# Kernel tuning notes

Measured on AMD Instinct MI355X. Metric: run time of the kernel, lower is better.

## Reference

```python
import jax, jax.numpy as jnp
import numpy as np

MAX_SEQ_LEN = 2048
H, K = 16, 8
D_IN, D_OUT = 1024, 1024
D_H, D_O = D_IN // H, D_OUT // H


def _get_phi(L, K):
    # Hankel matrix Z[i,j] = 2 / ((i+j)^3 - (i+j) + 1e-7), 1-indexed
    e = np.arange(1, L + 1, dtype=np.float64)
    s = e[:, None] + e[None, :]
    Z = 2.0 / (s ** 3 - s + 1e-7)
    sigma, phi = np.linalg.eigh(Z)
    sigma, phi = sigma[-K:], phi[:, -K:]
    phi = phi * sigma ** 0.25
    return jnp.asarray(phi, dtype=jnp.float32)  # (L, K)


def setup_inputs() -> dict:
    key = jax.random.key(0)
    k_x, k_w, k_d = jax.random.split(key, 3)
    B, T = 4, 2048
    x = jax.random.normal(k_x, (B, T, D_IN), dtype=jnp.float32)
    # kaiming_uniform(a=sqrt(5)) on (H,K,d_h,d_o): fan_in = K*d_h*d_o, bound = 1/sqrt(fan_in)
    fan_in = K * D_H * D_O
    bound = 1.0 / np.sqrt(fan_in)
    weight = jax.random.uniform(k_w, (H, K, D_H, D_O), minval=-bound, maxval=bound, dtype=jnp.float32)
    # torch init is zeros; use small random so the score path is exercised
    diag = 0.02 * jax.random.normal(k_d, (K, D_IN), dtype=jnp.float32)
    phi = _get_phi(MAX_SEQ_LEN, K)
    return {"x": x, "weight": weight, "diag": diag, "phi": phi}


def reference(x, weight, diag, phi):
    B, T, _ = x.shape
    Hh, Kk, d_h, d_o = weight.shape
    # scores: (B, T, K) = phi[:T] broadcast + x @ diag^T
    scores = phi[:T][None, :, :] + jnp.einsum('bti,ki->btk', x, diag)
    xh = x.reshape(B, T, Hh, d_h).transpose(0, 2, 1, 3)  # (B, H, T, d_h)
    # per-head, per-expert GEMM -> (B, H, K, T, d_o)
    y = jnp.einsum('bhti,hkio->bhkto', xh, weight)
    # score-weighted combine over experts -> (B, T, H, d_o)
    y = jnp.einsum('bhkto,btk->btho', y, scores)
    return y.reshape(B, T, Hh * d_o)
```

## Files before the change

### kernel.cpp

```cpp
#include <hip/hip_runtime.h>
#include <hip/hip_bf16.h>

#define BT    8192
#define SEQ_T 2048
#define DIN   1024
#define NH    16
#define NK    8
#define DH    64
#define DO    64
#define TT    256

typedef __bf16 bf16;
typedef __attribute__((ext_vector_type(8))) __bf16 bf16x8;
typedef __attribute__((ext_vector_type(4))) __bf16 bf16x4;
typedef __attribute__((ext_vector_type(4))) float floatx4;

__device__ inline void async_load16(const void* g, void* l) {
  __builtin_amdgcn_global_load_lds(
      (const __attribute__((address_space(1))) unsigned int*)g,
      (__attribute__((address_space(3))) unsigned int*)l, 16, 0, 0);
}

__global__ __launch_bounds__(256) void prep_kernel(
    const float* __restrict__ x, const float* __restrict__ weight,
    const float* __restrict__ diag, const float* __restrict__ phi,
    float* __restrict__ scores_t, bf16* __restrict__ wt)
{
  int blk = blockIdx.x, tid = threadIdx.x;
  if (blk < BT / 4) {
    int wave = tid >> 6, lane = tid & 63;
    int token = blk * 4 + wave;
    const floatx4* xr = (const floatx4*)(x + (size_t)token * DIN);
    const floatx4* dg = (const floatx4*)diag;
    floatx4 acc[NK];
#pragma unroll
    for (int k = 0; k < NK; k++) acc[k] = (floatx4){0.f, 0.f, 0.f, 0.f};
#pragma unroll
    for (int it = 0; it < 4; it++) {
      floatx4 xv = xr[it * 64 + lane];
#pragma unroll
      for (int k = 0; k < NK; k++) {
        floatx4 dv = dg[k * 256 + it * 64 + lane];
        acc[k] += xv * dv;
      }
    }
    float r[NK];
#pragma unroll
    for (int k = 0; k < NK; k++)
      r[k] = (acc[k][0] + acc[k][1]) + (acc[k][2] + acc[k][3]);
#pragma unroll
    for (int k = 0; k < NK; k++) {
      float v = r[k];
#pragma unroll
      for (int off = 32; off >= 1; off >>= 1) v += __shfl_xor(v, off, 64);
      r[k] = v;
    }
    if (lane == 0) {
      int t = token & (SEQ_T - 1);
#pragma unroll
      for (int k = 0; k < NK; k++)
        scores_t[(size_t)k * BT + token] = phi[t * NK + k] + r[k];
    }
  } else {
    __shared__ bf16 tile[64 * 68];
    int hk = blk - BT / 4;
    const float* wsrc = weight + (size_t)hk * DH * DO;
#pragma unroll
    for (int it = 0; it < 4; it++) {
      int idx = it * 1024 + tid * 4;
      int i = idx >> 6, o = idx & 63;
      floatx4 v = *(const floatx4*)(wsrc + idx);
#pragma unroll
      for (int r = 0; r < 4; r++)
        tile[(o + r) * 68 + i] = (bf16)v[r];
    }
    __syncthreads();
#pragma unroll
    for (int it = 0; it < 4; it++) {
      int idx = it * 1024 + tid * 4;
      int o2 = idx >> 6, i2 = idx & 63;
      bf16x4 v = *(const bf16x4*)&tile[o2 * 68 + i2];
      *(bf16x4*)(wt + (size_t)hk * 4096 + idx) = v;
    }
  }
}

__global__ __launch_bounds__(512, 4) void moe_kernel(
    const float* __restrict__ x, const bf16* __restrict__ wt,
    const float* __restrict__ scores_t, float* __restrict__ out)
{
  __shared__ char smem[NK * DO * DH * 2 + NK * TT * 4];
  bf16*  w_lds = (bf16*)smem;
  float* s_lds = (float*)(smem + NK * DO * DH * 2);

  int h  = blockIdx.x >> 5;
  int t0 = (blockIdx.x & 31) * TT;
  int tid = threadIdx.x, lane = tid & 63, w = tid >> 6;
  int l15 = lane & 15, q = lane >> 4;
  int R0 = (w >> 1) * 64;
  int C0 = (w & 1) * 32;

  const bf16* wh = wt + (size_t)h * NK * DO * DH;
#pragma unroll
  for (int it = 0; it < 8; it++) {
    int L = it * 512 + tid;
    int row = L >> 3, pc = L & 7;
    int lc = (pc - row) & 7;
    async_load16(wh + row * 64 + lc * 8,
                 (char*)w_lds + it * 8192 + w * 1024);
  }

  {
    int k = tid >> 6, t4 = (tid & 63) * 4;
    floatx4 sv = *(const floatx4*)(scores_t + (size_t)k * BT + t0 + t4);
    *(floatx4*)(s_lds + k * TT + t4) = sv;
  }

  bf16x8 a[4][2];
#pragma unroll
  for (int rb = 0; rb < 4; rb++) {
    int arow = t0 + R0 + rb * 16 + l15;
    const float* ap = x + (size_t)arow * DIN + h * DH;
#pragma unroll
    for (int ki = 0; ki < 2; ki++) {
      const floatx4* p = (const floatx4*)(ap + ki * 32 + q * 8);
      floatx4 f0 = p[0], f1 = p[1];
      bf16x8 av;
      av[0] = (bf16)f0[0]; av[1] = (bf16)f0[1];
      av[2] = (bf16)f0[2]; av[3] = (bf16)f0[3];
      av[4] = (bf16)f1[0]; av[5] = (bf16)f1[1];
      av[6] = (bf16)f1[2]; av[7] = (bf16)f1[3];
      a[rb][ki] = av;
    }
  }

  floatx4 y[4][2];
#pragma unroll
  for (int rb = 0; rb < 4; rb++)
#pragma unroll
    for (int nb = 0; nb < 2; nb++)
      y[rb][nb] = (floatx4){0.f, 0.f, 0.f, 0.f};

  __syncthreads();

#pragma unroll
  for (int k = 0; k < NK; k++) {
    bf16x8 b[2][2];
#pragma unroll
    for (int nb = 0; nb < 2; nb++) {
      int o = C0 + nb * 16 + l15;
      int row = k * 64 + o;
#pragma unroll
      for (int ki = 0; ki < 2; ki++) {
        int pc = (ki * 4 + q + o) & 7;
        b[nb][ki] = *(const bf16x8*)(w_lds + row * 64 + pc * 8);
      }
    }
    floatx4 s4[4];
#pragma unroll
    for (int rb = 0; rb < 4; rb++)
      s4[rb] = *(const floatx4*)(s_lds + k * TT + R0 + rb * 16 + q * 4);

#pragma unroll
    for (int rb = 0; rb < 4; rb++)
#pragma unroll
      for (int nb = 0; nb < 2; nb++) {
        floatx4 z = {0.f, 0.f, 0.f, 0.f};
        z = __builtin_amdgcn_mfma_f32_16x16x32_bf16(a[rb][0], b[nb][0], z, 0, 0, 0);
        z = __builtin_amdgcn_mfma_f32_16x16x32_bf16(a[rb][1], b[nb][1], z, 0, 0, 0);
#pragma unroll
        for (int r = 0; r < 4; r++)
          y[rb][nb][r] += s4[rb][r] * z[r];
      }
  }

#pragma unroll
  for (int rb = 0; rb < 4; rb++)
#pragma unroll
    for (int nb = 0; nb < 2; nb++) {
      int row = t0 + R0 + rb * 16 + q * 4;
      float* op = out + (size_t)row * (NH * DO) + h * DO + C0 + nb * 16 + l15;
#pragma unroll
      for (int r = 0; r < 4; r++)
        op[(size_t)r * (NH * DO)] = y[rb][nb][r];
    }
}

extern "C" void kernel_launch(void* const* d_in, const int* in_sizes, int n_in,
                              void* d_out, int out_size, void* d_ws, size_t ws_size,
                              hipStream_t stream) {
  const float* x      = (const float*)d_in[0];
  const float* weight = (const float*)d_in[1];
  const float* diag   = (const float*)d_in[2];
  const float* phi    = (const float*)d_in[3];
  float* out = (float*)d_out;

  bf16*  wt       = (bf16*)d_ws;
  float* scores_t = (float*)((char*)d_ws + (size_t)NH * NK * DH * DO * 2);

  prep_kernel<<<BT / 4 + NH * NK, 256, 0, stream>>>(x, weight, diag, phi, scores_t, wt);
  moe_kernel<<<NH * (BT / TT), 512, 0, stream>>>(x, wt, scores_t, out);
}
```

Before: 110.6 us.

## Keep expert weights in registers and stream token tiles with register double-buffering

The MoE kernel drops its LDS staging of weights and scores. Each 256-thread block now keeps its wave's slice of all eight expert weight matrices in registers, then walks 128 tokens in 32-token steps, prefetching the next x rows into a second register buffer while the current tile runs on MFMA. Scores are read straight from global memory. Blocks are ordered head-minor so neighbouring blocks share x rows. The prep kernel has each wave handle two tokens so the diag loads are reused. The aim is to cut LDS traffic and synchronisation and to overlap x loads with compute, at the cost of more registers and uncached score reads.

Result: slower. 133.8 us (+20.9%).

```diff
diff --git a/kernel.cpp b/kernel.cpp
--- a/kernel.cpp
+++ b/kernel.cpp
@@ -8,18 +8,11 @@
 #define NK    8
 #define DH    64
 #define DO    64
-#define TT    256
 
 typedef __bf16 bf16;
 typedef __attribute__((ext_vector_type(8))) __bf16 bf16x8;
 typedef __attribute__((ext_vector_type(4))) __bf16 bf16x4;
 typedef __attribute__((ext_vector_type(4))) float floatx4;
-
-__device__ inline void async_load16(const void* g, void* l) {
-  __builtin_amdgcn_global_load_lds(
-      (const __attribute__((address_space(1))) unsigned int*)g,
-      (__attribute__((address_space(3))) unsigned int*)l, 16, 0, 0);
-}
 
 __global__ __launch_bounds__(256) void prep_kernel(
     const float* __restrict__ x, const float* __restrict__ weight,
@@ -27,43 +20,56 @@
     float* __restrict__ scores_t, bf16* __restrict__ wt)
 {
   int blk = blockIdx.x, tid = threadIdx.x;
-  if (blk < BT / 4) {
+  if (blk < BT / 8) {
     int wave = tid >> 6, lane = tid & 63;
-    int token = blk * 4 + wave;
-    const floatx4* xr = (const floatx4*)(x + (size_t)token * DIN);
-    const floatx4* dg = (const floatx4*)diag;
-    floatx4 acc[NK];
+    int tok = blk * 8 + wave * 2;
+    const floatx4* xr0 = (const floatx4*)(x + (size_t)tok * DIN);
+    const floatx4* xr1 = (const floatx4*)(x + (size_t)(tok + 1) * DIN);
+    const floatx4* dg  = (const floatx4*)diag;
+    floatx4 a0[NK], a1[NK];
 #pragma unroll
-    for (int k = 0; k < NK; k++) acc[k] = (floatx4){0.f, 0.f, 0.f, 0.f};
+    for (int k = 0; k < NK; k++) {
+      a0[k] = (floatx4){0.f, 0.f, 0.f, 0.f};
+      a1[k] = (floatx4){0.f, 0.f, 0.f, 0.f};
+    }
 #pragma unroll
     for (int it = 0; it < 4; it++) {
-      floatx4 xv = xr[it * 64 + lane];
+      floatx4 xv0 = xr0[it * 64 + lane];
+      floatx4 xv1 = xr1[it * 64 + lane];
 #pragma unroll
       for (int k = 0; k < NK; k++) {
         floatx4 dv = dg[k * 256 + it * 64 + lane];
-        acc[k] += xv * dv;
+        a0[k] += xv0 * dv;
+        a1[k] += xv1 * dv;
       }
     }
-    float r[NK];
-#pragma unroll
-    for (int k = 0; k < NK; k++)
-      r[k] = (acc[k][0] + acc[k][1]) + (acc[k][2] + acc[k][3]);
+    float r0[NK], r1[NK];
 #pragma unroll
     for (int k = 0; k < NK; k++) {
-      float v = r[k];
+      r0[k] = (a0[k][0] + a0[k][1]) + (a0[k][2] + a0[k][3]);
+      r1[k] = (a1[k][0] + a1[k][1]) + (a1[k][2] + a1[k][3]);
+    }
 #pragma unroll
-      for (int off = 32; off >= 1; off >>= 1) v += __shfl_xor(v, off, 64);
-      r[k] = v;
+    for (int k = 0; k < NK; k++) {
+      float v0 = r0[k], v1 = r1[k];
+#pragma unroll
+      for (int off = 32; off >= 1; off >>= 1) {
+        v0 += __shfl_xor(v0, off, 64);
+        v1 += __shfl_xor(v1, off, 64);
+      }
+      r0[k] = v0; r1[k] = v1;
     }
     if (lane == 0) {
-      int t = token & (SEQ_T - 1);
+      int t = tok & (SEQ_T - 1);
 #pragma unroll
-      for (int k = 0; k < NK; k++)
-        scores_t[(size_t)k * BT + token] = phi[t * NK + k] + r[k];
+      for (int k = 0; k < NK; k++) {
+        scores_t[(size_t)k * BT + tok]     = phi[t * NK + k]       + r0[k];
+        scores_t[(size_t)k * BT + tok + 1] = phi[(t + 1) * NK + k] + r1[k];
+      }
     }
   } else {
     __shared__ bf16 tile[64 * 68];
-    int hk = blk - BT / 4;
+    int hk = blk - BT / 8;
     const float* wsrc = weight + (size_t)hk * DH * DO;
 #pragma unroll
     for (int it = 0; it < 4; it++) {
@@ -85,105 +91,92 @@
   }
 }
 
-__global__ __launch_bounds__(512, 4) void moe_kernel(
+__global__ __launch_bounds__(256) void moe_kernel(
     const float* __restrict__ x, const bf16* __restrict__ wt,
     const float* __restrict__ scores_t, float* __restrict__ out)
 {
-  __shared__ char smem[NK * DO * DH * 2 + NK * TT * 4];
-  bf16*  w_lds = (bf16*)smem;
-  float* s_lds = (float*)(smem + NK * DO * DH * 2);
-
-  int h  = blockIdx.x >> 5;
-  int t0 = (blockIdx.x & 31) * TT;
+  int g = blockIdx.x >> 4;
+  int h = blockIdx.x & (NH - 1);
   int tid = threadIdx.x, lane = tid & 63, w = tid >> 6;
   int l15 = lane & 15, q = lane >> 4;
-  int R0 = (w >> 1) * 64;
-  int C0 = (w & 1) * 32;
+  int C0 = w * 16;
+  int tg0 = g * 128;
 
-  const bf16* wh = wt + (size_t)h * NK * DO * DH;
+  bf16x8 b[NK][2];
+  {
+    const bf16* wh = wt + (size_t)h * NK * DO * DH;
 #pragma unroll
-  for (int it = 0; it < 8; it++) {
-    int L = it * 512 + tid;
-    int row = L >> 3, pc = L & 7;
-    int lc = (pc - row) & 7;
-    async_load16(wh + row * 64 + lc * 8,
-                 (char*)w_lds + it * 8192 + w * 1024);
-  }
-
-  {
-    int k = tid >> 6, t4 = (tid & 63) * 4;
-    floatx4 sv = *(const floatx4*)(scores_t + (size_t)k * BT + t0 + t4);
-    *(floatx4*)(s_lds + k * TT + t4) = sv;
-  }
-
-  bf16x8 a[4][2];
-#pragma unroll
-  for (int rb = 0; rb < 4; rb++) {
-    int arow = t0 + R0 + rb * 16 + l15;
-    const float* ap = x + (size_t)arow * DIN + h * DH;
-#pragma unroll
-    for (int ki = 0; ki < 2; ki++) {
-      const floatx4* p = (const floatx4*)(ap + ki * 32 + q * 8);
-      floatx4 f0 = p[0], f1 = p[1];
-      bf16x8 av;
-      av[0] = (bf16)f0[0]; av[1] = (bf16)f0[1];
-      av[2] = (bf16)f0[2]; av[3] = (bf16)f0[3];
-      av[4] = (bf16)f1[0]; av[5] = (bf16)f1[1];
-      av[6] = (bf16)f1[2]; av[7] = (bf16)f1[3];
-      a[rb][ki] = av;
+    for (int k = 0; k < NK; k++) {
+      const bf16* bp = wh + ((size_t)k * DO + C0 + l15) * DH + q * 8;
+      b[k][0] = *(const bf16x8*)bp;
+      b[k][1] = *(const bf16x8*)(bp + 32);
     }
   }
 
-  floatx4 y[4][2];
-#pragma unroll
-  for (int rb = 0; rb < 4; rb++)
-#pragma unroll
-    for (int nb = 0; nb < 2; nb++)
-      y[rb][nb] = (floatx4){0.f, 0.f, 0.f, 0.f};
-
-  __syncthreads();
+  const float* xc = x + (size_t)h * DH;
+  floatx4 af[2][2][2][2];
 
 #pragma unroll
-  for (int k = 0; k < NK; k++) {
-    bf16x8 b[2][2];
+  for (int rb = 0; rb < 2; rb++) {
+    const float* rp = xc + (size_t)(tg0 + rb * 16 + l15) * DIN;
 #pragma unroll
-    for (int nb = 0; nb < 2; nb++) {
-      int o = C0 + nb * 16 + l15;
-      int row = k * 64 + o;
-#pragma unroll
-      for (int ki = 0; ki < 2; ki++) {
-        int pc = (ki * 4 + q + o) & 7;
-        b[nb][ki] = *(const bf16x8*)(w_lds + row * 64 + pc * 8);
-      }
+    for (int ki = 0; ki < 2; ki++) {
+      const floatx4* p = (const floatx4*)(rp + ki * 32 + q * 8);
+      af[0][rb][ki][0] = p[0];
+      af[0][rb][ki][1] = p[1];
     }
-    floatx4 s4[4];
-#pragma unroll
-    for (int rb = 0; rb < 4; rb++)
-      s4[rb] = *(const floatx4*)(s_lds + k * TT + R0 + rb * 16 + q * 4);
-
-#pragma unroll
-    for (int rb = 0; rb < 4; rb++)
-#pragma unroll
-      for (int nb = 0; nb < 2; nb++) {
-        floatx4 z = {0.f, 0.f, 0.f, 0.f};
-        z = __builtin_amdgcn_mfma_f32_16x16x32_bf16(a[rb][0], b[nb][0], z, 0, 0, 0);
-        z = __builtin_amdgcn_mfma_f32_16x16x32_bf16(a[rb][1], b[nb][1], z, 0, 0, 0);
-#pragma unroll
-        for (int r = 0; r < 4; r++)
-          y[rb][nb][r] += s4[rb][r] * z[r];
-      }
   }
 
 #pragma unroll
-  for (int rb = 0; rb < 4; rb++)
+  for (int t = 0; t < 4; t++) {
+    int tr = tg0 + t * 32;
+    if (t < 3) {
 #pragma unroll
-    for (int nb = 0; nb < 2; nb++) {
-      int row = t0 + R0 + rb * 16 + q * 4;
-      float* op = out + (size_t)row * (NH * DO) + h * DO + C0 + nb * 16 + l15;
+      for (int rb = 0; rb < 2; rb++) {
+        const float* rp = xc + (size_t)(tr + 32 + rb * 16 + l15) * DIN;
 #pragma unroll
-      for (int r = 0; r < 4; r++)
-        op[(size_t)r * (NH * DO)] = y[rb][nb][r];
+        for (int ki = 0; ki < 2; ki++) {
+          const floatx4* p = (const floatx4*)(rp + ki * 32 + q * 8);
+          af[(t + 1) & 1][rb][ki][0] = p[0];
+          af[(t + 1) & 1][rb][ki][1] = p[1];
+        }
+      }
     }
+    bf16x8 a[2][2];
+#pragma unroll
+    for (int rb = 0; rb < 2; rb++)
+#pragma unroll
+      for (int ki = 0; ki < 2; ki++) {
+        floatx4 f0 = af[t & 1][rb][ki][0], f1 = af[t & 1][rb][ki][1];
+        bf16x8 av;
+        av[0] = (bf16)f0[0]; av[1] = (bf16)f0[1];
+        av[2] = (bf16)f0[2]; av[3] = (bf16)f0[3];
+        av[4] = (bf16)f1[0]; av[5] = (bf16)f1[1];
+        av[6] = (bf16)f1[2]; av[7] = (bf16)f1[3];
+        a[rb][ki] = av;
+      }
+
+    floatx4 y0 = (floatx4){0.f, 0.f, 0.f, 0.f};
+    floatx4 y1 = (floatx4){0.f, 0.f, 0.f, 0.f};
+#pragma unroll
+    for (int k = 0; k < NK; k++) {
+      floatx4 s0 = *(const floatx4*)(scores_t + (size_t)k * BT + tr + q * 4);
+      floatx4 s1 = *(const floatx4*)(scores_t + (size_t)k * BT + tr + 16 + q * 4);
+      floatx4 z0 = (floatx4){0.f, 0.f, 0.f, 0.f};
+      z0 = __builtin_amdgcn_mfma_f32_16x16x32_bf16(a[0][0], b[k][0], z0, 0, 0, 0);
+      z0 = __builtin_amdgcn_mfma_f32_16x16x32_bf16(a[0][1], b[k][1], z0, 0, 0, 0);
+      y0 += s0 * z0;
+      floatx4 z1 = (floatx4){0.f, 0.f, 0.f, 0.f};
+      z1 = __builtin_amdgcn_mfma_f32_16x16x32_bf16(a[1][0], b[k][0], z1, 0, 0, 0);
+      z1 = __builtin_amdgcn_mfma_f32_16x16x32_bf16(a[1][1], b[k][1], z1, 0, 0, 0);
+      y1 += s1 * z1;
+    }
+#pragma unroll
+    for (int r = 0; r < 4; r++) {
+      out[(size_t)(tr + q * 4 + r) * (NH * DO) + h * DO + C0 + l15]      = y0[r];
+      out[(size_t)(tr + 16 + q * 4 + r) * (NH * DO) + h * DO + C0 + l15] = y1[r];
+    }
+  }
 }
 
 extern "C" void kernel_launch(void* const* d_in, const int* in_sizes, int n_in,
@@ -198,6 +191,6 @@
   bf16*  wt       = (bf16*)d_ws;
   float* scores_t = (float*)((char*)d_ws + (size_t)NH * NK * DH * DO * 2);
 
-  prep_kernel<<<BT / 4 + NH * NK, 256, 0, stream>>>(x, weight, diag, phi, scores_t, wt);
-  moe_kernel<<<NH * (BT / TT), 512, 0, stream>>>(x, wt, scores_t, out);
+  prep_kernel<<<BT / 8 + NH * NK, 256, 0, stream>>>(x, weight, diag, phi, scores_t, wt);
+  moe_kernel<<<64 * NH, 256, 0, stream>>>(x, wt, scores_t, out);
 }
```
